# Kernel optimization log

Hardware: AMD Instinct MI355X
Metric: run time of the kernel (lower is better)

Reference implementation:

```python
import jax, jax.numpy as jnp
import numpy as np

NX, NY, NT = 256, 256, 10          # N = [nx, ny, nt]
DX = DY = DZ = 20e-9               # dr (cell size, m)
DT = 5e-12                         # dt (s)
TIMESTEPS = 3000
F0 = 6.0e9                         # drive frequency (hard-coded in module)
MU0 = 4.0 * np.pi * 1e-7
CPW_XPOS = np.array([40, 48, 56, 64, 112, 120, 128, 136, 184, 192, 200, 208], dtype=np.int32)
CPW_ZPOS = 100e-9                  # scalar z offset of the CPW plane
NFIL = CPW_XPOS.shape[0]

_x = jnp.arange(NX, dtype=jnp.float32) * DX
_y = jnp.arange(NY, dtype=jnp.float32) * DY
XG, YG = jnp.meshgrid(_x, _y, indexing="ij")          # [nx, ny]
XFIL = _x[CPW_XPOS]                                    # [nfil]
DX2_FIL = (XG[None] - XFIL[:, None, None]) ** 2        # [nfil, nx, ny]


def setup_inputs() -> dict:
    key = jax.random.key(0)
    m = 0.02 * jax.random.normal(key, (NT, 3, NX, NY), dtype=jnp.float32)
    Msat = jnp.float32(8.0e5)      # saturation magnetization (A/m)
    return {"m": m, "Msat": Msat}


def _curl_y(Mx, Mz):
    # y-component of curl(M): dMx/dz - dMz/dx (numpy.gradient-style finite diffs)
    dMx_dz = jnp.gradient(Mx, axis=2) / DZ
    dMz_dx = jnp.gradient(Mz, axis=0) / DX
    return dMx_dz - dMz_dx         # [nx, ny, 2]


def _vector_potential_y(curl_y):
    # A_y at targets (i in cpw_xpos, all j) via Biot-Savart sum over the grid.
    # The distance does not depend on the duplicated z layer, so sum curl over z first.
    S = curl_y.sum(axis=2)                                      # [nx, ny]
    z2 = jnp.float32(CPW_ZPOS) ** 2

    def a_for_row(yj):                                          # one pickup y, all filaments
        dist = jnp.sqrt(DX2_FIL + (YG - yj)[None] ** 2 + z2)    # [nfil, nx, ny]
        frac = jnp.nan_to_num(S[None] / dist)
        return frac.sum(axis=(1, 2))                            # [nfil]

    a = jax.lax.map(a_for_row, _y)                              # [ny, nfil]
    return (MU0 / (4.0 * np.pi) * DX * DY * DZ) * a.T           # [nfil, ny]


def reference(m, Msat):
    def a_y_at(m_t):                                            # m_t: [3, nx, ny]
        M = m_t * Msat
        Mx = jnp.repeat(M[0][:, :, None], 2, axis=2)            # torch.cat((m_, m_), 2)
        Mz = jnp.repeat(M[2][:, :, None], 2, axis=2)
        return _vector_potential_y(_curl_y(Mx, Mz))

    A_all = jax.lax.map(a_y_at, m)                              # [nt, nfil, ny]
    # deltaV[t-1, f] = -sum_y(E_y) * dy with E_y = -(A_y - A_y_prev) / dt
    deltaV = (A_all[1:] - A_all[:-1]).sum(axis=2) * (DY / DT)   # [nt-1, nfil]

    t = jnp.arange(TIMESTEPS - NT + 1, TIMESTEPS, dtype=jnp.float32) * DT  # [nt-1]
    sin_vec = jnp.sin(2.0 * np.pi * F0 * t)
    cos_vec = jnp.cos(2.0 * np.pi * F0 * t)
    L = t.shape[0]
    norm = DT * F0 * 2.0 * np.pi / (np.pi * (L * DT * F0))      # == 2/L, kept literal
    re = jnp.sum(cos_vec[:, None] * deltaV, axis=0) * norm      # [nfil]
    im = jnp.sum(sin_vec[:, None] * deltaV, axis=0) * norm      # [nfil]
    ffit = cos_vec[:, None] * re[None, :] + sin_vec[:, None] * im[None, :]
    return deltaV, ffit
```

## Files before the change

### kernel.cpp

```cpp
#include <hip/hip_runtime.h>
#include <math.h>

#define GRID    65536
#define NFIL    12
#define NTm1    9
#define UMAX    216
#define GROUPS  64
#define RPG     4
#define NBLK2   (NTm1 * GROUPS)

static constexpr double PI_d = 3.14159265358979323846;

__constant__ int c_xpos[NFIL] = {40,48,56,64,112,120,128,136,184,192,200,208};

__global__ __launch_bounds__(256) void build_Ktab(float* __restrict__ Kt) {
    const int u    = blockIdx.x * 4 + (threadIdx.x >> 6);
    const int lane = threadIdx.x & 63;
    if (u >= UMAX) return;

    const double dxv = (double)u * 20e-9;
    const double r2  = dxv * dxv + 1e-14;

    double g[4], P[4];
#pragma unroll
    for (int e = 0; e < 4; ++e) {
        const double dy = (double)(4 * lane + e) * 20e-9;
        g[e] = 1.0 / sqrt(r2 + dy * dy);
    }
    P[0] = g[0]; P[1] = P[0] + g[1]; P[2] = P[1] + g[2]; P[3] = P[2] + g[3];

    const double lsum = P[3];
    double scan = lsum;
#pragma unroll
    for (int off = 1; off < 64; off <<= 1) {
        const double v = __shfl_up(scan, off, 64);
        if (lane >= off) scan += v;
    }
    const double excl = scan - lsum;
#pragma unroll
    for (int e = 0; e < 4; ++e) P[e] += excl;

    double rev[4];
#pragma unroll
    for (int e = 0; e < 4; ++e)
        rev[e] = __shfl(P[3 - e], 63 - lane, 64);

    const double g0 = 1.0 / sqrt(r2);
    float4 o;
    o.x = (float)(P[0] + rev[0] - g0);
    o.y = (float)(P[1] + rev[1] - g0);
    o.z = (float)(P[2] + rev[2] - g0);
    o.w = (float)(P[3] + rev[3] - g0);
    *(float4*)(Kt + (u << 8) + 4 * lane) = o;
}

__global__ __launch_bounds__(256) void fused_dot(const float* __restrict__ m,
                                                 const float* __restrict__ Kt,
                                                 double* __restrict__ partials) {
    const int k = blockIdx.x / GROUPS;
    const int g = blockIdx.x % GROUPS;
    const int j = threadIdx.x;

    const float* mz0 = m + (size_t)(3 * k + 2) * GRID;
    const float* mz1 = m + (size_t)(3 * k + 5) * GRID;

    const int base = g * RPG;
    float d[6];
#pragma unroll
    for (int r = 0; r < 6; ++r) {
        int row = base - 1 + r;
        row = row < 0 ? 0 : (row > 255 ? 255 : row);
        d[r] = mz1[row * 256 + j] - mz0[row * 256 + j];
    }

    double acc[NFIL];
#pragma unroll
    for (int f = 0; f < NFIL; ++f) acc[f] = 0.0;

#pragma unroll
    for (int r = 0; r < RPG; ++r) {
        const int i = base + r;
        const int im_idx = (i == 0   ? 0   : i - 1) - base + 1;
        const int ip_idx = (i == 255 ? 255 : i + 1) - base + 1;
        const float sc = (i == 0 || i == 255) ? 1.0f : 0.5f;
        const double dmd = (double)(sc * (d[ip_idx] - d[im_idx]));
#pragma unroll
        for (int f = 0; f < NFIL; ++f) {
            const int u = abs(i - c_xpos[f]);
            acc[f] = fma(dmd, (double)Kt[(u << 8) + j], acc[f]);
        }
    }

    __shared__ double lds[4][NFIL];
    const int lane = threadIdx.x & 63, wid = threadIdx.x >> 6;
#pragma unroll
    for (int f = 0; f < NFIL; ++f) {
        double v = acc[f];
        for (int off = 32; off > 0; off >>= 1)
            v += __shfl_down(v, off, 64);
        if (lane == 0) lds[wid][f] = v;
    }
    __syncthreads();
    if (threadIdx.x < NFIL)
        partials[(size_t)blockIdx.x * NFIL + threadIdx.x] =
            lds[0][threadIdx.x] + lds[1][threadIdx.x] +
            lds[2][threadIdx.x] + lds[3][threadIdx.x];
}

__global__ __launch_bounds__(128) void finalize(const double* __restrict__ partials,
                                                const float* __restrict__ msat_p,
                                                float* __restrict__ out) {
    __shared__ double cs[NTm1], sn[NTm1], re[NFIL], im[NFIL], dV[NTm1 * NFIL];
    const int t = threadIdx.x;
    if (t < NTm1) {
        const double tt = (double)(2991 + t) * 5e-12;
        const double ph = 2.0 * PI_d * 6.0e9 * tt;
        cs[t] = cos(ph);
        sn[t] = sin(ph);
    }
    if (t < NTm1 * NFIL) {
        const int kk = t / NFIL, f = t - NFIL * kk;
        double s = 0.0;
        for (int gg = 0; gg < GROUPS; ++gg)
            s += partials[(size_t)(kk * GROUPS + gg) * NFIL + f];
        const double msat = (double)msat_p[0];
        const double coef = -2.0 * msat * 1e-7 * (20e-9) * (20e-9) * (20e-9) / 5e-12;
        dV[t] = coef * s;
    }
    __syncthreads();
    if (t < NFIL) {
        double r = 0.0, s = 0.0;
        for (int kk = 0; kk < NTm1; ++kk) {
            const double v = dV[kk * NFIL + t];
            r += cs[kk] * v;
            s += sn[kk] * v;
        }
        re[t] = r * (2.0 / 9.0);
        im[t] = s * (2.0 / 9.0);
    }
    __syncthreads();
    if (t < NTm1 * NFIL) {
        out[t] = (float)dV[t];
        const int kk = t / NFIL, f = t - NFIL * kk;
        out[NTm1 * NFIL + t] = (float)(cs[kk] * re[f] + sn[kk] * im[f]);
    }
}

extern "C" void kernel_launch(void* const* d_in, const int* in_sizes, int n_in,
                              void* d_out, int out_size, void* d_ws, size_t ws_size,
                              hipStream_t stream) {
    (void)in_sizes; (void)n_in; (void)out_size; (void)ws_size;
    const float* m      = (const float*)d_in[0];
    const float* msat_p = (const float*)d_in[1];
    float* out = (float*)d_out;

    char* ws = (char*)d_ws;
    float*  Kt       = (float*)ws;
    size_t  off      = ((size_t)UMAX * 256 * sizeof(float) + 255) & ~(size_t)255;
    double* partials = (double*)(ws + off);

    build_Ktab<<<(UMAX + 3) / 4, 256, 0, stream>>>(Kt);
    fused_dot <<<NBLK2, 256, 0, stream>>>(m, Kt, partials);
    finalize  <<<1, 128, 0, stream>>>(partials, msat_p, out);
}
```

Before: 67.01 us.

## Fold symmetric kernel columns and split filaments across waves in fused_dot

The lookup table is symmetric in j, so each thread now pre-adds the finite-difference values at j and 255-j (staged through shared memory) and multiplies the sum by one table entry, halving table loads and fp64 FMAs. Each of the four waves now owns three filaments instead of all twelve. That removes the per-filament shared-memory cross-wave reduction: each wave reduces with shuffles and writes its partials directly. The cost is one extra __syncthreads and a shared-memory staging buffer, and correctness depends on the table staying exactly symmetric.

```diff
diff --git a/kernel.cpp b/kernel.cpp
--- a/kernel.cpp
+++ b/kernel.cpp
@@ -60,51 +60,69 @@
     const int k = blockIdx.x / GROUPS;
     const int g = blockIdx.x % GROUPS;
     const int j = threadIdx.x;
+    const int wid  = threadIdx.x >> 6;
+    const int lane = threadIdx.x & 63;
 
     const float* mz0 = m + (size_t)(3 * k + 2) * GRID;
     const float* mz1 = m + (size_t)(3 * k + 5) * GRID;
+    const int base = g * RPG;
 
-    const int base = g * RPG;
-    float d[6];
+    __shared__ float dmd_s[RPG][256];
+
+    float d[RPG + 2];
 #pragma unroll
-    for (int r = 0; r < 6; ++r) {
+    for (int r = 0; r < RPG + 2; ++r) {
         int row = base - 1 + r;
         row = row < 0 ? 0 : (row > 255 ? 255 : row);
         d[r] = mz1[row * 256 + j] - mz0[row * 256 + j];
     }
-
-    double acc[NFIL];
-#pragma unroll
-    for (int f = 0; f < NFIL; ++f) acc[f] = 0.0;
-
 #pragma unroll
     for (int r = 0; r < RPG; ++r) {
         const int i = base + r;
         const int im_idx = (i == 0   ? 0   : i - 1) - base + 1;
         const int ip_idx = (i == 255 ? 255 : i + 1) - base + 1;
         const float sc = (i == 0 || i == 255) ? 1.0f : 0.5f;
-        const double dmd = (double)(sc * (d[ip_idx] - d[im_idx]));
+        dmd_s[r][j] = sc * (d[ip_idx] - d[im_idx]);
+    }
+
+    float kv[2][RPG][3];
 #pragma unroll
-        for (int f = 0; f < NFIL; ++f) {
-            const int u = abs(i - c_xpos[f]);
-            acc[f] = fma(dmd, (double)Kt[(u << 8) + j], acc[f]);
+    for (int c = 0; c < 2; ++c) {
+        const int jA = c * 64 + lane;
+#pragma unroll
+        for (int r = 0; r < RPG; ++r) {
+            const int i = base + r;
+#pragma unroll
+            for (int ff = 0; ff < 3; ++ff) {
+                const int u = abs(i - c_xpos[3 * wid + ff]);
+                kv[c][r][ff] = Kt[(u << 8) + jA];
+            }
+        }
+    }
+    __syncthreads();
+
+    double acc[3] = {0.0, 0.0, 0.0};
+#pragma unroll
+    for (int c = 0; c < 2; ++c) {
+        const int jA = c * 64 + lane;
+        const int jB = 255 - jA;
+#pragma unroll
+        for (int r = 0; r < RPG; ++r) {
+            const double ds2 = (double)(dmd_s[r][jA] + dmd_s[r][jB]);
+#pragma unroll
+            for (int ff = 0; ff < 3; ++ff)
+                acc[ff] = fma(ds2, (double)kv[c][r][ff], acc[ff]);
         }
     }
 
-    __shared__ double lds[4][NFIL];
-    const int lane = threadIdx.x & 63, wid = threadIdx.x >> 6;
 #pragma unroll
-    for (int f = 0; f < NFIL; ++f) {
-        double v = acc[f];
+    for (int ff = 0; ff < 3; ++ff) {
+        double v = acc[ff];
         for (int off = 32; off > 0; off >>= 1)
             v += __shfl_down(v, off, 64);
-        if (lane == 0) lds[wid][f] = v;
+        if (lane == 0)
+            partials[(size_t)blockIdx.x * NFIL + 3 * wid + ff] = v;
     }
-    __syncthreads();
-    if (threadIdx.x < NFIL)
-        partials[(size_t)blockIdx.x * NFIL + threadIdx.x] =
-            lds[0][threadIdx.x] + lds[1][threadIdx.x] +
-            lds[2][threadIdx.x] + lds[3][threadIdx.x];
 }
 
 __global__ __launch_bounds__(128) void finalize(const double* __restrict__ partials,
```

New measurement: 64.36 us. 1.04x faster.
